# Optimization experiments

Measured on AMD Instinct MI355X. Metric: run time of the kernel, lower is better.

## Reference

```python
import jax, jax.numpy as jnp
import numpy as np

B, T, C, H, HD = 4, 2048, 1024, 16, 64

def setup_inputs() -> dict:
    key = jax.random.key(0)
    ks = jax.random.split(key, 9)
    s = 1.0 / np.sqrt(C)
    return {
        "x":  jax.random.normal(ks[0], (B, T, C), jnp.float32),
        "Wq": jax.random.normal(ks[1], (H, C, HD), jnp.float32) * s,
        "bq": jax.random.normal(ks[2], (H, HD), jnp.float32) * 0.02,
        "Wk": jax.random.normal(ks[3], (H, C, HD), jnp.float32) * s,
        "bk": jax.random.normal(ks[4], (H, HD), jnp.float32) * 0.02,
        "Wv": jax.random.normal(ks[5], (H, C, HD), jnp.float32) * s,
        "bv": jax.random.normal(ks[6], (H, HD), jnp.float32) * 0.02,
        "Wo": jax.random.normal(ks[7], (C, C), jnp.float32) * s,
        "bo": jax.random.normal(ks[8], (C,), jnp.float32) * 0.02,
    }

def reference(x, Wq, bq, Wk, bk, Wv, bv, Wo, bo):
    # Batched per-head linear projections: [B,T,C] x [H,C,D] -> [B,H,T,D]
    q = jnp.einsum('btc,hcd->bhtd', x, Wq) + bq[None, :, None, :]
    k = jnp.einsum('btc,hcd->bhtd', x, Wk) + bk[None, :, None, :]
    v = jnp.einsum('btc,hcd->bhtd', x, Wv) + bv[None, :, None, :]
    scale = 1.0 / jnp.sqrt(jnp.asarray(HD, q.dtype))
    scores = jnp.einsum('bhtd,bhsd->bhts', q, k) * scale  # [B,H,T,T]
    causal = jnp.tril(jnp.ones((T, T), dtype=bool))
    scores = jnp.where(causal[None, None, :, :], scores, -jnp.inf)
    attn = jax.nn.softmax(scores, axis=-1)
    out = jnp.einsum('bhts,bhsd->bhtd', attn, v)          # [B,H,T,D]
    concat = out.transpose(0, 2, 1, 3).reshape(B, T, C)   # concat heads
    return concat @ Wo + bo
```

## Files before the change

### kernel.cpp

```cpp
#include <hip/hip_runtime.h>
#include <stdint.h>

#define TSEQ 2048
#define NHEAD 16

typedef __attribute__((ext_vector_type(8))) short bf16x8;
typedef __attribute__((ext_vector_type(4))) short bf16x4;
typedef __attribute__((ext_vector_type(4))) float f32x4;

__device__ __forceinline__ unsigned short f2bf(float f) {
  union { float f; uint32_t u; } c;
  c.f = f;
  uint32_t u = c.u;
  u += 0x7fffu + ((u >> 16) & 1u);
  return (unsigned short)(u >> 16);
}

__device__ __forceinline__ float fexp2(float x) {
#if __has_builtin(__builtin_amdgcn_exp2f)
  return __builtin_amdgcn_exp2f(x);
#else
  return __builtin_exp2f(x);
#endif
}

using as3_void  = __attribute__((address_space(3))) void;
using as1_cvoid = const __attribute__((address_space(1))) void;

__device__ __forceinline__ void gld_lds16(const void* g, void* l) {
  __builtin_amdgcn_global_load_lds((as1_cvoid*)g, (as3_void*)l, 16, 0, 0);
}


__global__ void cast_x_kernel(const float4* __restrict__ x, unsigned short* __restrict__ xb) {
  int i = blockIdx.x * 256 + threadIdx.x;
  float4 v = x[i];
  int e = i * 4;
  int m = e >> 10, k = e & 1023;
  int ks = k ^ ((m & 7) << 3);
  ushort4 o;
  o.x = f2bf(v.x); o.y = f2bf(v.y); o.z = f2bf(v.z); o.w = f2bf(v.w);
  *(ushort4*)(xb + (size_t)m * 1024 + ks) = o;
}

__global__ void repack_wqkv(const float* __restrict__ Wq, const float* __restrict__ Wk,
                            const float* __restrict__ Wv, unsigned short* __restrict__ BT) {
  __shared__ unsigned short tile[64][72];
  const float* W = (blockIdx.z == 0) ? Wq : (blockIdx.z == 1) ? Wk : Wv;
  const int h = blockIdx.y;
  const int c0 = blockIdx.x * 64;
  const int t = threadIdx.x;
  const float* src = W + ((size_t)h * 1024 + c0) * 64;
#pragma unroll
  for (int p = 0; p < 16; ++p) {
    int idx = p * 256 + t;
    int cc = idx >> 6, d = idx & 63;
    tile[cc][d] = f2bf(src[(size_t)cc * 64 + d]);
  }
  __syncthreads();
  unsigned short* dst = BT + ((size_t)blockIdx.z * 1024 + (size_t)h * 64) * 1024 + c0;
#pragma unroll
  for (int p = 0; p < 16; ++p) {
    int idx = p * 256 + t;
    int d = idx >> 6, cc = idx & 63;
    dst[(size_t)d * 1024 + (cc ^ ((d & 7) << 3))] = tile[cc][d];
  }
}

__global__ void repack_wo(const float* __restrict__ Wo, unsigned short* __restrict__ WoT) {
  __shared__ unsigned short tile[64][72];
  const int k0 = blockIdx.x * 64;
  const int n0 = blockIdx.y * 64;
  const int t = threadIdx.x;
#pragma unroll
  for (int p = 0; p < 16; ++p) {
    int idx = p * 256 + t;
    int kk = idx >> 6, nn = idx & 63;
    tile[kk][nn] = f2bf(Wo[(size_t)(k0 + kk) * 1024 + n0 + nn]);
  }
  __syncthreads();
#pragma unroll
  for (int p = 0; p < 16; ++p) {
    int idx = p * 256 + t;
    int nn = idx >> 6, kk = idx & 63;
    WoT[(size_t)(n0 + nn) * 1024 + k0 + (kk ^ ((nn & 7) << 3))] = tile[kk][nn];
  }
}


template <int MODE>
__global__ __launch_bounds__(256) void gemm_bt(
    const unsigned short* __restrict__ A, const unsigned short* __restrict__ BTm,
    const float* __restrict__ bias0, const float* __restrict__ bias1,
    const float* __restrict__ bias2,
    unsigned short* __restrict__ qo, unsigned short* __restrict__ ko,
    unsigned short* __restrict__ vto, float* __restrict__ outf,
    int K, int N) {
  __shared__ __align__(16) char lds[65536];

  const int tid = threadIdx.x, lane = tid & 63, wv = tid >> 6;
  const int wr = wv >> 1, wc = wv & 1;
  const int g = lane >> 4, r = lane & 15;
  const int m0 = blockIdx.x * 128, n0 = blockIdx.y * 128;
  const int xr = (r & 7) << 4;

  f32x4 acc[4][4] = {};

  const int arow = tid >> 3;
  const int acol = (tid & 7) * 8;
  const unsigned short* Ab = A + (size_t)(m0 + arow) * K + acol;
  const unsigned short* Bb = BTm + (size_t)(n0 + arow) * K + acol;

#define GSTAGE(b, kel) do {                                                 \
    char* ab_ = lds + (b) * 32768 + wv * 1024;                              \
    _Pragma("unroll") for (int i = 0; i < 4; ++i) {                         \
      gld_lds16(Ab + (size_t)i * 32 * K + (kel), ab_ + i * 4096);           \
      gld_lds16(Bb + (size_t)i * 32 * K + (kel), ab_ + 16384 + i * 4096);   \
    } } while (0)

  const int NT = K >> 6;
  GSTAGE(0, 0);
  __syncthreads();

  for (int t = 0; t < NT; ++t) {
    const int cur = t & 1;
    if (t + 1 < NT) GSTAGE(cur ^ 1, (t + 1) << 6);
    const char* Ar = lds + cur * 32768;
    const char* Br = Ar + 16384;
#pragma unroll
    for (int kk = 0; kk < 2; ++kk) {
      bf16x8 af[4], bfv[4];
#pragma unroll
      for (int f = 0; f < 4; ++f) {
        af[f]  = *(const bf16x8*)(Ar + (wr * 64 + f * 16 + r) * 128 + ((kk * 64 + g * 16) ^ xr));
        bfv[f] = *(const bf16x8*)(Br + (wc * 64 + f * 16 + r) * 128 + ((kk * 64 + g * 16) ^ xr));
      }
#pragma unroll
      for (int fm = 0; fm < 4; ++fm)
#pragma unroll
        for (int fn = 0; fn < 4; ++fn)
          acc[fm][fn] = __builtin_amdgcn_mfma_f32_16x16x32_bf16(af[fm], bfv[fn], acc[fm][fn], 0, 0, 0);
    }
    __syncthreads();
  }
#undef GSTAGE

  if (MODE == 0) {
    const int which = n0 >> 10;
    const float* bias = (which == 0) ? bias0 : (which == 1) ? bias1 : bias2;
    const float sc = (which == 0) ? 0.18033688011112042f : 1.0f;
    const int b = m0 >> 11;
    const int t0 = m0 & 2047;
    const int hb0 = (n0 & 1023) >> 6;
    unsigned short* ep = (unsigned short*)lds;

    __syncthreads();
    if (which == 2) {
#pragma unroll
      for (int fn = 0; fn < 4; ++fn) {
        const int dg = wc * 64 + fn * 16 + r;
        const float bvl = bias[(hb0 + (dg >> 6)) * 64 + (dg & 63)];
#pragma unroll
        for (int fm = 0; fm < 4; ++fm)
#pragma unroll
          for (int j = 0; j < 4; ++j) {
            const int t = wr * 64 + fm * 16 + 4 * g + j;
            ep[dg * 136 + t] = f2bf(acc[fm][fn][j] + bvl);
          }
      }
    } else {
#pragma unroll
      for (int fn = 0; fn < 4; ++fn) {
        const int dg = wc * 64 + fn * 16 + r;
        const float bvl = bias[(hb0 + (dg >> 6)) * 64 + (dg & 63)];
#pragma unroll
        for (int fm = 0; fm < 4; ++fm)
#pragma unroll
          for (int j = 0; j < 4; ++j) {
            const int t = wr * 64 + fm * 16 + 4 * g + j;
            ep[t * 136 + dg] = f2bf((acc[fm][fn][j] + bvl) * sc);
          }
      }
    }
    __syncthreads();
    if (which == 2) {
#pragma unroll
      for (int p = 0; p < 8; ++p) {
        const int idx = p * 256 + tid;
        const int dg = idx >> 4, u = idx & 15;
        const int head = hb0 + (dg >> 6), d = dg & 63;
        const size_t bhb = (size_t)(b * NHEAD + head) * 131072;
        const int c = u >> 3, w = u & 7;
        const int base_t = c * 64 + (w >> 2) * 32 + (w & 3) * 4;
        union { bf16x4 h4[2]; bf16x8 v8; } cc2;
        cc2.h4[0] = *(const bf16x4*)(ep + dg * 136 + base_t);
        cc2.h4[1] = *(const bf16x4*)(ep + dg * 136 + base_t + 16);
        *(bf16x8*)(vto + bhb + (size_t)((t0 >> 6) + c) * 4096 + (size_t)d * 64 +
                   ((w * 8) ^ ((d & 7) << 3))) = cc2.v8;
      }
    } else {
      unsigned short* qk = (which == 1) ? ko : qo;
#pragma unroll
      for (int p = 0; p < 8; ++p) {
        const int idx = p * 256 + tid;
        const int row = idx >> 4, seg = idx & 15;
        const int head = hb0 + (seg >> 3);
        const size_t bhb = (size_t)(b * NHEAD + head) * 131072;
        const bf16x8 v8 = *(const bf16x8*)(ep + row * 136 + seg * 8);
        const int tt = t0 + row;
        int dbase = (seg & 7) * 8;
        if (which == 1) dbase ^= (tt & 7) << 3;
        *(bf16x8*)(qk + bhb + (size_t)tt * 64 + dbase) = v8;
      }
    }
  } else {
    float* epf = (float*)lds;
#pragma unroll
    for (int h = 0; h < 2; ++h) {
      __syncthreads();
      if (wc == h) {
#pragma unroll
        for (int fn = 0; fn < 4; ++fn) {
          const int n = n0 + h * 64 + fn * 16 + r;
          const float bvl = bias0[n];
#pragma unroll
          for (int fm = 0; fm < 4; ++fm)
#pragma unroll
            for (int j = 0; j < 4; ++j)
              epf[(wr * 64 + fm * 16 + 4 * g + j) * 68 + fn * 16 + r] = acc[fm][fn][j] + bvl;
        }
      }
      __syncthreads();
#pragma unroll
      for (int p = 0; p < 8; ++p) {
        const int row = p * 16 + (tid >> 4);
        const int seg = tid & 15;
        const f32x4 v4 = *(const f32x4*)(epf + row * 68 + seg * 4);
        *(f32x4*)(outf + (size_t)(m0 + row) * N + n0 + h * 64 + seg * 4) = v4;
      }
    }
  }
}


__global__ __launch_bounds__(256) void attn_fwd(const unsigned short* __restrict__ Qm,
                                                const unsigned short* __restrict__ Km,
                                                const unsigned short* __restrict__ Vtm,
                                                unsigned short* __restrict__ Om) {
  __shared__ __align__(16) unsigned short Ks[2][4096];
  __shared__ __align__(16) unsigned short Vs[2][4096];

  const int tid = threadIdx.x, lane = tid & 63, wv = tid >> 6;
  const int g = lane >> 4, r = lane & 15;
  const int bh = blockIdx.x & 63;
  const int p = 31 - (blockIdx.x >> 6);
  const int nt = p + 1;

  const unsigned short* Qp = Qm + (size_t)bh * 131072;
  const unsigned short* Kp = Km + (size_t)bh * 131072;
  const unsigned short* Vp = Vtm + (size_t)bh * 131072;

  const int qb = p * 64 + wv * 16;

  bf16x8 qf[2];
#pragma unroll
  for (int h2 = 0; h2 < 2; ++h2)
    qf[h2] = *(const bf16x8*)(Qp + (size_t)(qb + r) * 64 + h2 * 32 + g * 8);

  f32x4 oacc[4] = {};
  f32x4 lacc = {};
  const short oneb = (short)0x3F80;
  const bf16x8 vones = {oneb, oneb, oneb, oneb, oneb, oneb, oneb, oneb};

  const uint32_t sw = (uint32_t)((r & 7) << 4);
  const uint32_t ob = (uint32_t)(r * 128);
  const uint32_t c0 = ((uint32_t)(g * 16)) ^ sw;
  const uint32_t c1 = ((uint32_t)(64 + g * 16)) ^ sw;
  const char* const KsB = (const char*)Ks;
  const char* const VsB = (const char*)Vs;

#define ASTAGE(buf, c) do {                                                      \
    const unsigned short* kg_ = Kp + (size_t)(c) * 4096;                         \
    const unsigned short* vg_ = Vp + (size_t)(c) * 4096;                         \
    const int o0_ = wv * 1024;                                                   \
    gld_lds16(kg_ + (o0_ >> 1) + lane * 8, (char*)Ks[buf] + o0_);                \
    gld_lds16(vg_ + (o0_ >> 1) + lane * 8, (char*)Vs[buf] + o0_);                \
    gld_lds16(kg_ + ((o0_ + 4096) >> 1) + lane * 8, (char*)Ks[buf] + o0_ + 4096);\
    gld_lds16(vg_ + ((o0_ + 4096) >> 1) + lane * 8, (char*)Vs[buf] + o0_ + 4096);\
  } while (0)

  ASTAGE(0, 0);
  __syncthreads();

  for (int t = 0; t < nt; ++t) {
    const uint32_t bo = (uint32_t)((t & 1) << 13);
    if (t + 1 < nt) ASTAGE((t & 1) ^ 1, t + 1);

    const char* pk0 = KsB + bo + ob + c0;
    const char* pk1 = KsB + bo + ob + c1;
    const char* pv0 = VsB + bo + ob + c0;
    const char* pv1 = VsB + bo + ob + c1;
    bf16x8 kf[4][2], vf[4][2];
#pragma unroll
    for (int tt = 0; tt < 4; ++tt) {
      kf[tt][0] = *(const bf16x8*)(pk0 + tt * 2048);
      kf[tt][1] = *(const bf16x8*)(pk1 + tt * 2048);
      vf[tt][0] = *(const bf16x8*)(pv0 + tt * 2048);
      vf[tt][1] = *(const bf16x8*)(pv1 + tt * 2048);
    }

    f32x4 sT[4];
    __builtin_amdgcn_s_setprio(1);
#pragma unroll
    for (int tt = 0; tt < 4; ++tt) {
      f32x4 a = {0.f, 0.f, 0.f, 0.f};
      a = __builtin_amdgcn_mfma_f32_16x16x32_bf16(kf[tt][0], qf[0], a, 0, 0, 0);
      a = __builtin_amdgcn_mfma_f32_16x16x32_bf16(kf[tt][1], qf[1], a, 0, 0, 0);
      sT[tt] = a;
    }
    __builtin_amdgcn_s_setprio(0);

    const int qg = qb + r;
    if (t * 64 + 63 > qb) {
#pragma unroll
      for (int tt = 0; tt < 4; ++tt)
#pragma unroll
        for (int j = 0; j < 4; ++j) {
          const int kv = t * 64 + tt * 16 + 4 * g + j;
          sT[tt][j] = (kv <= qg) ? sT[tt][j] : -__builtin_inff();
        }
    }

#pragma unroll
    for (int tt = 0; tt < 4; ++tt)
#pragma unroll
      for (int j = 0; j < 4; ++j)
        sT[tt][j] = fexp2(sT[tt][j]);

    union { uint32_t w[8]; bf16x8 v[2]; } pu;
#pragma unroll
    for (int tt = 0; tt < 4; ++tt) {
      asm("v_cvt_pk_bf16_f32 %0, %1, %2" : "=v"(pu.w[2 * tt])
          : "v"(sT[tt][0]), "v"(sT[tt][1]));
      asm("v_cvt_pk_bf16_f32 %0, %1, %2" : "=v"(pu.w[2 * tt + 1])
          : "v"(sT[tt][2]), "v"(sT[tt][3]));
    }

    __builtin_amdgcn_s_setprio(1);
#pragma unroll
    for (int kk = 0; kk < 2; ++kk) {
#pragma unroll
      for (int df = 0; df < 4; ++df)
        oacc[df] = __builtin_amdgcn_mfma_f32_16x16x32_bf16(pu.v[kk], vf[df][kk], oacc[df], 0, 0, 0);
      lacc = __builtin_amdgcn_mfma_f32_16x16x32_bf16(pu.v[kk], vones, lacc, 0, 0, 0);
    }
    __builtin_amdgcn_s_setprio(0);

    __syncthreads();
  }
#undef ASTAGE

  const int b = bh >> 4, h = bh & 15;
  float inv[4];
#pragma unroll
  for (int j = 0; j < 4; ++j) inv[j] = __builtin_amdgcn_rcpf(lacc[j]);
#pragma unroll
  for (int df = 0; df < 4; ++df)
#pragma unroll
    for (int j = 0; j < 4; ++j) {
      const int trow = qb + 4 * g + j;
      const float ov = oacc[df][j] * inv[j];
      const int col = (df * 16 + r) ^ ((trow & 7) << 3);
      Om[((size_t)(b * TSEQ + trow)) * 1024 + h * 64 + col] = f2bf(ov);
    }
}


extern "C" void kernel_launch(void* const* d_in, const int* in_sizes, int n_in,
                              void* d_out, int out_size, void* d_ws, size_t ws_size,
                              hipStream_t stream) {
  const float* x  = (const float*)d_in[0];
  const float* Wq = (const float*)d_in[1];
  const float* bq = (const float*)d_in[2];
  const float* Wk = (const float*)d_in[3];
  const float* bk = (const float*)d_in[4];
  const float* Wv = (const float*)d_in[5];
  const float* bv = (const float*)d_in[6];
  const float* Wo = (const float*)d_in[7];
  const float* bo = (const float*)d_in[8];
  float* out = (float*)d_out;

  unsigned short* xb  = (unsigned short*)d_ws;
  unsigned short* btq = xb + (size_t)8192 * 1024;
  unsigned short* wot = btq + (size_t)3072 * 1024;
  unsigned short* qb  = wot + (size_t)1024 * 1024;
  unsigned short* kb  = qb + (size_t)64 * 2048 * 64;
  unsigned short* vtb = kb + (size_t)64 * 2048 * 64;

  cast_x_kernel<<<8192, 256, 0, stream>>>((const float4*)x, xb);
  repack_wqkv<<<dim3(16, 16, 3), 256, 0, stream>>>(Wq, Wk, Wv, btq);
  repack_wo<<<dim3(16, 16), 256, 0, stream>>>(Wo, wot);

  gemm_bt<0><<<dim3(64, 24), 256, 0, stream>>>(xb, btq, bq, bk, bv, qb, kb, vtb,
                                               nullptr, 1024, 3072);
  attn_fwd<<<2048, 256, 0, stream>>>(qb, kb, vtb, xb);
  gemm_bt<1><<<dim3(64, 8), 256, 0, stream>>>(xb, wot, bo, nullptr, nullptr,
                                              nullptr, nullptr, nullptr, out,
                                              1024, 1024);
}
```

Measured before the change: 166.6 us.

## Process two query tiles per attention block and merge prep kernels

The attention kernel now handles 128 query rows per block: two 64-row sub-tiles share each staged K/V tile in LDS, which halves K/V global traffic and the block count. A sub-tile skips a KV tile when that tile lies entirely beyond its causal range. The three preprocessing kernels (x cast, Wqkv repack, Wo repack) are merged into one launch with branches on block index, removing two launch gaps. Risks include higher register pressure from doubled accumulators and Q fragments, and fewer blocks (1024) for load balancing under causal imbalance.

Result: no change. 164.3 us (median of 2 runs) (-1.4%).

```diff
diff --git a/kernel.cpp b/kernel.cpp
--- a/kernel.cpp
+++ b/kernel.cpp
@@ -32,58 +32,58 @@
 }
 
 
-__global__ void cast_x_kernel(const float4* __restrict__ x, unsigned short* __restrict__ xb) {
-  int i = blockIdx.x * 256 + threadIdx.x;
-  float4 v = x[i];
-  int e = i * 4;
-  int m = e >> 10, k = e & 1023;
-  int ks = k ^ ((m & 7) << 3);
-  ushort4 o;
-  o.x = f2bf(v.x); o.y = f2bf(v.y); o.z = f2bf(v.z); o.w = f2bf(v.w);
-  *(ushort4*)(xb + (size_t)m * 1024 + ks) = o;
-}
-
-__global__ void repack_wqkv(const float* __restrict__ Wq, const float* __restrict__ Wk,
-                            const float* __restrict__ Wv, unsigned short* __restrict__ BT) {
+__global__ void prep_all(const float* __restrict__ x,
+                         const float* __restrict__ Wq, const float* __restrict__ Wk,
+                         const float* __restrict__ Wv, const float* __restrict__ Wo,
+                         unsigned short* __restrict__ xb, unsigned short* __restrict__ BT,
+                         unsigned short* __restrict__ WoT) {
   __shared__ unsigned short tile[64][72];
-  const float* W = (blockIdx.z == 0) ? Wq : (blockIdx.z == 1) ? Wk : Wv;
-  const int h = blockIdx.y;
-  const int c0 = blockIdx.x * 64;
+  const int bidx = blockIdx.x;
   const int t = threadIdx.x;
-  const float* src = W + ((size_t)h * 1024 + c0) * 64;
-#pragma unroll
-  for (int p = 0; p < 16; ++p) {
-    int idx = p * 256 + t;
-    int cc = idx >> 6, d = idx & 63;
-    tile[cc][d] = f2bf(src[(size_t)cc * 64 + d]);
-  }
-  __syncthreads();
-  unsigned short* dst = BT + ((size_t)blockIdx.z * 1024 + (size_t)h * 64) * 1024 + c0;
-#pragma unroll
-  for (int p = 0; p < 16; ++p) {
-    int idx = p * 256 + t;
-    int d = idx >> 6, cc = idx & 63;
-    dst[(size_t)d * 1024 + (cc ^ ((d & 7) << 3))] = tile[cc][d];
-  }
-}
-
-__global__ void repack_wo(const float* __restrict__ Wo, unsigned short* __restrict__ WoT) {
-  __shared__ unsigned short tile[64][72];
-  const int k0 = blockIdx.x * 64;
-  const int n0 = blockIdx.y * 64;
-  const int t = threadIdx.x;
-#pragma unroll
-  for (int p = 0; p < 16; ++p) {
-    int idx = p * 256 + t;
-    int kk = idx >> 6, nn = idx & 63;
-    tile[kk][nn] = f2bf(Wo[(size_t)(k0 + kk) * 1024 + n0 + nn]);
-  }
-  __syncthreads();
-#pragma unroll
-  for (int p = 0; p < 16; ++p) {
-    int idx = p * 256 + t;
-    int nn = idx >> 6, kk = idx & 63;
-    WoT[(size_t)(n0 + nn) * 1024 + k0 + (kk ^ ((nn & 7) << 3))] = tile[kk][nn];
+  if (bidx < 8192) {
+    const int i = bidx * 256 + t;
+    float4 v = ((const float4*)x)[i];
+    int e = i * 4;
+    int m = e >> 10, k = e & 1023;
+    int ks = k ^ ((m & 7) << 3);
+    ushort4 o;
+    o.x = f2bf(v.x); o.y = f2bf(v.y); o.z = f2bf(v.z); o.w = f2bf(v.w);
+    *(ushort4*)(xb + (size_t)m * 1024 + ks) = o;
+  } else if (bidx < 8960) {
+    const int bb = bidx - 8192;
+    const int c0 = (bb & 15) * 64, h = (bb >> 4) & 15, z = bb >> 8;
+    const float* W = (z == 0) ? Wq : (z == 1) ? Wk : Wv;
+    const float* src = W + ((size_t)h * 1024 + c0) * 64;
+#pragma unroll
+    for (int p = 0; p < 16; ++p) {
+      int idx = p * 256 + t;
+      int cc = idx >> 6, d = idx & 63;
+      tile[cc][d] = f2bf(src[(size_t)cc * 64 + d]);
+    }
+    __syncthreads();
+    unsigned short* dst = BT + ((size_t)z * 1024 + (size_t)h * 64) * 1024 + c0;
+#pragma unroll
+    for (int p = 0; p < 16; ++p) {
+      int idx = p * 256 + t;
+      int d = idx >> 6, cc = idx & 63;
+      dst[(size_t)d * 1024 + (cc ^ ((d & 7) << 3))] = tile[cc][d];
+    }
+  } else {
+    const int bb = bidx - 8960;
+    const int k0 = (bb & 15) * 64, n0 = (bb >> 4) * 64;
+#pragma unroll
+    for (int p = 0; p < 16; ++p) {
+      int idx = p * 256 + t;
+      int kk = idx >> 6, nn = idx & 63;
+      tile[kk][nn] = f2bf(Wo[(size_t)(k0 + kk) * 1024 + n0 + nn]);
+    }
+    __syncthreads();
+#pragma unroll
+    for (int p = 0; p < 16; ++p) {
+      int idx = p * 256 + t;
+      int nn = idx >> 6, kk = idx & 63;
+      WoT[(size_t)(n0 + nn) * 1024 + k0 + (kk ^ ((nn & 7) << 3))] = tile[kk][nn];
+    }
   }
 }
 
@@ -253,22 +253,24 @@
   const int tid = threadIdx.x, lane = tid & 63, wv = tid >> 6;
   const int g = lane >> 4, r = lane & 15;
   const int bh = blockIdx.x & 63;
-  const int p = 31 - (blockIdx.x >> 6);
-  const int nt = p + 1;
+  const int qp = 15 - (blockIdx.x >> 6);
+  const int nt = qp * 2 + 2;
 
   const unsigned short* Qp = Qm + (size_t)bh * 131072;
   const unsigned short* Kp = Km + (size_t)bh * 131072;
   const unsigned short* Vp = Vtm + (size_t)bh * 131072;
 
-  const int qb = p * 64 + wv * 16;
-
-  bf16x8 qf[2];
-#pragma unroll
-  for (int h2 = 0; h2 < 2; ++h2)
-    qf[h2] = *(const bf16x8*)(Qp + (size_t)(qb + r) * 64 + h2 * 32 + g * 8);
-
-  f32x4 oacc[4] = {};
-  f32x4 lacc = {};
+  const int qb[2] = {qp * 128 + wv * 16, qp * 128 + 64 + wv * 16};
+
+  bf16x8 qf[2][2];
+#pragma unroll
+  for (int mi = 0; mi < 2; ++mi)
+#pragma unroll
+    for (int h2 = 0; h2 < 2; ++h2)
+      qf[mi][h2] = *(const bf16x8*)(Qp + (size_t)(qb[mi] + r) * 64 + h2 * 32 + g * 8);
+
+  f32x4 oacc[2][4] = {};
+  f32x4 lacc[2] = {};
   const short oneb = (short)0x3F80;
   const bf16x8 vones = {oneb, oneb, oneb, oneb, oneb, oneb, oneb, oneb};
 
@@ -309,70 +311,78 @@
       vf[tt][1] = *(const bf16x8*)(pv1 + tt * 2048);
     }
 
-    f32x4 sT[4];
-    __builtin_amdgcn_s_setprio(1);
-#pragma unroll
-    for (int tt = 0; tt < 4; ++tt) {
-      f32x4 a = {0.f, 0.f, 0.f, 0.f};
-      a = __builtin_amdgcn_mfma_f32_16x16x32_bf16(kf[tt][0], qf[0], a, 0, 0, 0);
-      a = __builtin_amdgcn_mfma_f32_16x16x32_bf16(kf[tt][1], qf[1], a, 0, 0, 0);
-      sT[tt] = a;
-    }
-    __builtin_amdgcn_s_setprio(0);
-
-    const int qg = qb + r;
-    if (t * 64 + 63 > qb) {
+#pragma unroll
+    for (int mi = 0; mi < 2; ++mi) {
+      const int qbm = qb[mi];
+      if (t * 64 > qbm + 15) continue;
+
+      f32x4 sT[4];
+      __builtin_amdgcn_s_setprio(1);
+#pragma unroll
+      for (int tt = 0; tt < 4; ++tt) {
+        f32x4 a = {0.f, 0.f, 0.f, 0.f};
+        a = __builtin_amdgcn_mfma_f32_16x16x32_bf16(kf[tt][0], qf[mi][0], a, 0, 0, 0);
+        a = __builtin_amdgcn_mfma_f32_16x16x32_bf16(kf[tt][1], qf[mi][1], a, 0, 0, 0);
+        sT[tt] = a;
+      }
+      __builtin_amdgcn_s_setprio(0);
+
+      const int qg = qbm + r;
+      if (t * 64 + 63 > qbm) {
+#pragma unroll
+        for (int tt = 0; tt < 4; ++tt)
+#pragma unroll
+          for (int j = 0; j < 4; ++j) {
+            const int kv = t * 64 + tt * 16 + 4 * g + j;
+            sT[tt][j] = (kv <= qg) ? sT[tt][j] : -__builtin_inff();
+          }
+      }
+
 #pragma unroll
       for (int tt = 0; tt < 4; ++tt)
 #pragma unroll
-        for (int j = 0; j < 4; ++j) {
-          const int kv = t * 64 + tt * 16 + 4 * g + j;
-          sT[tt][j] = (kv <= qg) ? sT[tt][j] : -__builtin_inff();
-        }
-    }
-
-#pragma unroll
-    for (int tt = 0; tt < 4; ++tt)
-#pragma unroll
-      for (int j = 0; j < 4; ++j)
-        sT[tt][j] = fexp2(sT[tt][j]);
-
-    union { uint32_t w[8]; bf16x8 v[2]; } pu;
-#pragma unroll
-    for (int tt = 0; tt < 4; ++tt) {
-      asm("v_cvt_pk_bf16_f32 %0, %1, %2" : "=v"(pu.w[2 * tt])
-          : "v"(sT[tt][0]), "v"(sT[tt][1]));
-      asm("v_cvt_pk_bf16_f32 %0, %1, %2" : "=v"(pu.w[2 * tt + 1])
-          : "v"(sT[tt][2]), "v"(sT[tt][3]));
-    }
-
-    __builtin_amdgcn_s_setprio(1);
-#pragma unroll
-    for (int kk = 0; kk < 2; ++kk) {
-#pragma unroll
-      for (int df = 0; df < 4; ++df)
-        oacc[df] = __builtin_amdgcn_mfma_f32_16x16x32_bf16(pu.v[kk], vf[df][kk], oacc[df], 0, 0, 0);
-      lacc = __builtin_amdgcn_mfma_f32_16x16x32_bf16(pu.v[kk], vones, lacc, 0, 0, 0);
-    }
-    __builtin_amdgcn_s_setprio(0);
-
+        for (int j = 0; j < 4; ++j)
+          sT[tt][j] = fexp2(sT[tt][j]);
+
+      union { uint32_t w[8]; bf16x8 v[2]; } pu;
+#pragma unroll
+      for (int tt = 0; tt < 4; ++tt) {
+        asm("v_cvt_pk_bf16_f32 %0, %1, %2" : "=v"(pu.w[2 * tt])
+            : "v"(sT[tt][0]), "v"(sT[tt][1]));
+        asm("v_cvt_pk_bf16_f32 %0, %1, %2" : "=v"(pu.w[2 * tt + 1])
+            : "v"(sT[tt][2]), "v"(sT[tt][3]));
+      }
+
+      __builtin_amdgcn_s_setprio(1);
+#pragma unroll
+      for (int kk = 0; kk < 2; ++kk) {
+#pragma unroll
+        for (int df = 0; df < 4; ++df)
+          oacc[mi][df] = __builtin_amdgcn_mfma_f32_16x16x32_bf16(pu.v[kk], vf[df][kk], oacc[mi][df], 0, 0, 0);
+        lacc[mi] = __builtin_amdgcn_mfma_f32_16x16x32_bf16(pu.v[kk], vones, lacc[mi], 0, 0, 0);
+      }
+      __builtin_amdgcn_s_setprio(0);
+    }
     __syncthreads();
   }
 #undef ASTAGE
 
   const int b = bh >> 4, h = bh & 15;
-  float inv[4];
-#pragma unroll
-  for (int j = 0; j < 4; ++j) inv[j] = __builtin_amdgcn_rcpf(lacc[j]);
-#pragma unroll
-  for (int df = 0; df < 4; ++df)
-#pragma unroll
-    for (int j = 0; j < 4; ++j) {
-      const int trow = qb + 4 * g + j;
-      const float ov = oacc[df][j] * inv[j];
-      const int col = (df * 16 + r) ^ ((trow & 7) << 3);
-      Om[((size_t)(b * TSEQ + trow)) * 1024 + h * 64 + col] = f2bf(ov);
-    }
+#pragma unroll
+  for (int mi = 0; mi < 2; ++mi) {
+    float inv[4];
+#pragma unroll
+    for (int j = 0; j < 4; ++j) inv[j] = __builtin_amdgcn_rcpf(lacc[mi][j]);
+#pragma unroll
+    for (int df = 0; df < 4; ++df)
+#pragma unroll
+      for (int j = 0; j < 4; ++j) {
+        const int trow = qb[mi] + 4 * g + j;
+        const float ov = oacc[mi][df][j] * inv[j];
+        const int col = (df * 16 + r) ^ ((trow & 7) << 3);
+        Om[((size_t)(b * TSEQ + trow)) * 1024 + h * 64 + col] = f2bf(ov);
+      }
+  }
 }
 
 
@@ -397,13 +407,11 @@
   unsigned short* kb  = qb + (size_t)64 * 2048 * 64;
   unsigned short* vtb = kb + (size_t)64 * 2048 * 64;
 
-  cast_x_kernel<<<8192, 256, 0, stream>>>((const float4*)x, xb);
-  repack_wqkv<<<dim3(16, 16, 3), 256, 0, stream>>>(Wq, Wk, Wv, btq);
-  repack_wo<<<dim3(16, 16), 256, 0, stream>>>(Wo, wot);
+  prep_all<<<9216, 256, 0, stream>>>(x, Wq, Wk, Wv, Wo, xb, btq, wot);
 
   gemm_bt<0><<<dim3(64, 24), 256, 0, stream>>>(xb, btq, bq, bk, bv, qb, kb, vtb,
                                                nullptr, 1024, 3072);
-  attn_fwd<<<2048, 256, 0, stream>>>(qb, kb, vtb, xb);
+  attn_fwd<<<1024, 256, 0, stream>>>(qb, kb, vtb, xb);
   gemm_bt<1><<<dim3(64, 8), 256, 0, stream>>>(xb, wot, bo, nullptr, nullptr,
                                               nullptr, nullptr, nullptr, out,
                                               1024, 1024);
```
